# Kernel optimization log

Measured on AMD Instinct MI355X. Metric: run time of the kernel, lower is better.

Reference implementation:

```python
import jax, jax.numpy as jnp
import numpy as np

B, L, D, H, T = 1024, 50, 4, 512, 30


def _lstm_cell(x, h, c, W_ih, W_hh, b_ih, b_hh):
    # PyTorch LSTM gate order: i, f, g, o
    g = x @ W_ih.T + b_ih + h @ W_hh.T + b_hh
    i, f, gg, o = jnp.split(g, 4, axis=-1)
    c = jax.nn.sigmoid(f) * c + jax.nn.sigmoid(i) * jnp.tanh(gg)
    h = jax.nn.sigmoid(o) * jnp.tanh(c)
    return h, c


def setup_inputs() -> dict:
    key = jax.random.key(0)
    ks = jax.random.split(key, 16)
    s = 0.05
    return {
        "input_tensor": jax.random.normal(ks[0], (B, L, D), jnp.float32),
        "target_len": T,
        "enc_W_ih": jax.random.normal(ks[1], (4 * H, D), jnp.float32) * s,
        "enc_W_hh": jax.random.normal(ks[2], (4 * H, H), jnp.float32) * s,
        "enc_b_ih": jax.random.normal(ks[3], (4 * H,), jnp.float32) * s,
        "enc_b_hh": jax.random.normal(ks[4], (4 * H,), jnp.float32) * s,
        "attn_W": jax.random.normal(ks[5], (L, H + D), jnp.float32) * s,
        "attn_b": jax.random.normal(ks[6], (L,), jnp.float32) * s,
        "comb_W": jax.random.normal(ks[7], (H, H + D), jnp.float32) * s,
        "comb_b": jax.random.normal(ks[8], (H,), jnp.float32) * s,
        "dec_W_ih": jax.random.normal(ks[9], (4 * H, H), jnp.float32) * s,
        "dec_W_hh": jax.random.normal(ks[10], (4 * H, H), jnp.float32) * s,
        "dec_b_ih": jax.random.normal(ks[11], (4 * H,), jnp.float32) * s,
        "dec_b_hh": jax.random.normal(ks[12], (4 * H,), jnp.float32) * s,
        "out_W": jax.random.normal(ks[13], (D, H), jnp.float32) * s,
        "out_b": jax.random.normal(ks[14], (D,), jnp.float32) * s,
    }


def reference(input_tensor, target_len, enc_W_ih, enc_W_hh, enc_b_ih, enc_b_hh,
              attn_W, attn_b, comb_W, comb_b,
              dec_W_ih, dec_W_hh, dec_b_ih, dec_b_hh, out_W, out_b):
    b = input_tensor.shape[0]

    # ---- encoder LSTM over input_len steps ----
    def enc_step(carry, x_t):
        h, c = carry
        h, c = _lstm_cell(x_t, h, c, enc_W_ih, enc_W_hh, enc_b_ih, enc_b_hh)
        return (h, c), h

    h0 = jnp.zeros((b, H), input_tensor.dtype)
    (h_enc, c_enc), enc_hs = jax.lax.scan(enc_step, (h0, h0),
                                          jnp.swapaxes(input_tensor, 0, 1))
    encoder_outputs = jnp.swapaxes(enc_hs, 0, 1)  # [B, L, H]

    # ---- recursive attention decoder over target_len steps ----
    def dec_step(carry, _):
        h, c, x = carry
        # faithful to torch: h.reshape(h.shape[1], -1).transpose(1, 0)
        h_r = jnp.transpose(h.reshape(H, -1))  # [B, H] (memory reinterpret)
        attn_logits = jnp.concatenate([x, h_r], axis=1) @ attn_W.T + attn_b
        attn_weights = jax.nn.softmax(attn_logits, axis=1)        # [B, L]
        attn_applied = jnp.einsum('bl,blh->bh', attn_weights, encoder_outputs)
        comb = jnp.concatenate([x, attn_applied], axis=1) @ comb_W.T + comb_b
        comb = jax.nn.relu(comb)                                  # [B, H]
        h, c = _lstm_cell(comb, h, c, dec_W_ih, dec_W_hh, dec_b_ih, dec_b_hh)
        pred = h @ out_W.T + out_b                                # [B, D]
        return (h, c, pred), pred

    dec_in0 = input_tensor[:, -1, :]
    _, preds = jax.lax.scan(dec_step, (h_enc, c_enc, dec_in0), None,
                            length=target_len)
    return jnp.swapaxes(preds, 0, 1)  # [B, target_len, D]
```

## Files before the change

### kernel.cpp

```cpp
#include <hip/hip_runtime.h>
#include <hip/hip_bf16.h>

#define Bsz   1024
#define Lseq  50
#define Din   4
#define Hd    512
#define Tlen  30
#define NWG   256

typedef __hip_bfloat16 bf16;
typedef short s16x8 __attribute__((ext_vector_type(8)));
typedef short s16x4 __attribute__((ext_vector_type(4)));
typedef float f32x4 __attribute__((ext_vector_type(4)));

__device__ __forceinline__ float bf2f(bf16 x){ return __bfloat162float(x); }
__device__ __forceinline__ bf16  f2bf(float x){ return __float2bfloat16(x); }
__device__ __forceinline__ float bfbits2f(short u){
    union { unsigned int ui; float f; } v;
    v.ui = ((unsigned int)(unsigned short)u) << 16;
    return v.f;
}
__device__ __forceinline__ short f2bfbits(float x){
    bf16 h = f2bf(x); short s; __builtin_memcpy(&s, &h, 2); return s;
}
__device__ __forceinline__ float sigm(float x){ return 1.0f/(1.0f + __expf(-x)); }

#define OFF_ABUF0   (0u)
#define OFF_ABUF1   (2u<<20)
#define OFF_ATTNAP  (8u<<20)
#define OFF_XDEC    (9u<<20)
#define OFF_FLAG    ((9u<<20) + (16u<<10))
#define OFF_CNT     ((9u<<20) + (20u<<10))
#define OFF_COMBWR  ((9u<<20) + (32u<<10))
#define OFF_ATTNWR  ((9u<<20) + (600u<<10))
#define OFF_WCACHE  (10u<<20)
#define OFF_ENCOUT  (18u<<20)

#define WC_INPUT 0
#define WC_EWIH  204800
#define WC_EWHH  212992
#define WC_EBIH  1261568
#define WC_EBHH  1263616
#define WC_AW    1265664
#define WC_AB    1291464
#define WC_CW    1291520
#define WC_CB    1555712
#define WC_DWIH  1556224
#define WC_DWHH  2604800
#define WC_DBIH  3653376
#define WC_DBHH  3655424
#define WC_OW    3657472
#define WC_OB    3659520
#define WC_TOTAL 3659524

__device__ __constant__ int WOFF[15] = {
    WC_INPUT, WC_EWIH, WC_EWHH, WC_EBIH, WC_EBHH, WC_AW, WC_AB, WC_CW,
    WC_CB, WC_DWIH, WC_DWHH, WC_DBIH, WC_DBHH, WC_OW, WC_OB };
__device__ __constant__ int WNUM[15] = {
    204800, 8192, 1048576, 2048, 2048, 25800, 50, 264192,
    512, 1048576, 1048576, 2048, 2048, 2048, 4 };

struct Ptrs15 { const void* p[15]; };

__global__ void probe_kernel(const unsigned int* __restrict__ w, int* flag){
    __shared__ int cnt;
    if (threadIdx.x == 0) cnt = 0;
    __syncthreads();
    int c = 0;
    for (int i = threadIdx.x; i < 4096; i += 256){
        unsigned e = (w[i] >> 7) & 0xFFu;
        c += (e >= 0x80u) ? 1 : 0;
    }
    atomicAdd(&cnt, c);
    __syncthreads();
    if (threadIdx.x == 0) *flag = (cnt > 400) ? 1 : 0;
}

__global__ __launch_bounds__(256) void convert_kernel(
    Ptrs15 srcs, const int* __restrict__ flag, bf16* __restrict__ dst)
{
    const int f = *flag;
    for (int idx = blockIdx.x*256 + threadIdx.x; idx < WC_TOTAL;
         idx += gridDim.x*256){
        int a = 0;
#pragma unroll
        for (int j = 1; j < 15; ++j) if (idx >= WOFF[j]) a = j;
        const int local = idx - WOFF[a];
        if (local >= WNUM[a]) continue;
        bf16 v;
        if (f) v = f2bf(((const float*)srcs.p[a])[local]);
        else   v = ((const bf16*)srcs.p[a])[local];
        dst[idx] = v;
    }
}

__global__ __launch_bounds__(256) void setup_kernel(
    bf16* __restrict__ Abuf0, bf16* __restrict__ Abuf1,
    bf16* __restrict__ combWr, bf16* __restrict__ attnWr,
    const bf16* __restrict__ cWc, const bf16* __restrict__ aWc)
{
    const unsigned idx = blockIdx.x*256u + threadIdx.x;
    if (idx < (unsigned)Bsz*Hd){
        const unsigned row = idx >> 9, col = idx & (Hd-1);
        const bf16 z = f2bf(0.0f);
        Abuf0[(size_t)row*1024 + Hd + col] = z;
        Abuf1[(size_t)row*1024 + Hd + col] = z;
    }
    if (idx < (unsigned)Hd*Hd)
        combWr[idx] = cWc[(size_t)(idx >> 9)*(Hd+Din) + Din + (idx & (Hd-1))];
    if (idx < (unsigned)Lseq*Hd)
        attnWr[idx] = aWc[(size_t)(idx >> 9)*(Hd+Din) + Din + (idx & (Hd-1))];
}

struct MegaP {
    const bf16 *input, *eWih, *eWhh, *ebih, *ebhh;
    const bf16 *aW, *ab, *cW, *cb, *dWih, *dWhh, *dbih, *dbhh, *oW, *ob;
    const bf16 *combWr, *attnWr;
    bf16 *A0, *A1, *encout, *attnap, *xdec;
    int *cntg, *cntl, *xccmap;
    const int *flag;
    void *dout;
};

__global__ __launch_bounds__(512, 2) void mega_kernel(MegaP P)
{
    __shared__ short whh_lds[128*520];
    __shared__ float hr_s[4][Hd];
    __shared__ float ctx_s[2][4][Hd];
    __shared__ float aw_s[4][64];
    __shared__ int   xmap_s[NWG];
    __shared__ int   info_s[4];

    const int wg = blockIdx.x, tid = threadIdx.x;
    const int wave = tid >> 6, lane = tid & 63;
    const int quad = lane >> 4, l15 = lane & 15;
    const int lbase = lane & ~3;
    const int f32out = *P.flag;

    int epg = 0;
    int eplc = 0;

    if (tid == 0){
        int xcc = 0;
        asm volatile("s_getreg_b32 %0, hwreg(HW_REG_XCC_ID)" : "=s"(xcc));
        P.xccmap[wg] = xcc & 7;
    }

    auto GBAR = [&](){
        ++epg;
        __syncthreads();
        if (tid == 0){
            __threadfence();
            __hip_atomic_fetch_add(P.cntg, 1, __ATOMIC_RELEASE, __HIP_MEMORY_SCOPE_AGENT);
            while (__hip_atomic_load(P.cntg, __ATOMIC_RELAXED, __HIP_MEMORY_SCOPE_AGENT) < epg*NWG)
                __builtin_amdgcn_s_sleep(1);
            (void)__hip_atomic_load(P.cntg, __ATOMIC_ACQUIRE, __HIP_MEMORY_SCOPE_AGENT);
        }
        __syncthreads();
    };

    GBAR();

    if (tid < NWG) xmap_s[tid] = P.xccmap[tid];
    __syncthreads();
    if (tid == 0){
        int cnt8[8] = {0,0,0,0,0,0,0,0};
        const int myx = xmap_s[wg];
        int rank = 0;
        for (int i = 0; i < NWG; ++i){
            cnt8[xmap_s[i]]++;
            if (i < wg && xmap_s[i] == myx) rank++;
        }
        int bal = 1;
        for (int i = 0; i < 8; ++i) bal &= (cnt8[i] == 32);
        info_s[0] = bal ? myx  : (wg >> 5);
        info_s[1] = bal ? rank : (wg & 31);
        info_s[2] = bal;
    }
    __syncthreads();
    const int xcd = info_s[0], slot = info_s[1], bal = info_s[2];

    int* cntl = P.cntl + xcd*16;
    auto LBAR = [&](){
        if (!bal){ GBAR(); return; }
        ++eplc;
        __syncthreads();
        if (tid == 0){
            atomicAdd(cntl, 1);
            while (__hip_atomic_load(cntl, __ATOMIC_RELAXED, __HIP_MEMORY_SCOPE_AGENT) < eplc*32)
                __builtin_amdgcn_s_sleep(1);
        }
        __syncthreads();
        asm volatile("buffer_inv" ::: "memory");
    };

    bf16* bufs[2] = { P.A0, P.A1 };

    const int mtl = slot >> 4, ntl = slot & 15;
    const int bm0 = xcd*128 + mtl*64, hc0 = ntl*32;
    const int wm = wave >> 2, wn = wave & 3;
    const int arow0 = bm0 + wm*32 + l15;

    int ng[2];
#pragma unroll
    for (int nf = 0; nf < 2; ++nf){
        const int n = wn*32 + nf*16 + l15;
        ng[nf] = (n & 3)*Hd + hc0 + (n >> 2);
    }

    float bias_e[2], wxv_e[2][4];
#pragma unroll
    for (int nf = 0; nf < 2; ++nf){
        bias_e[nf] = bf2f(P.ebih[ng[nf]]) + bf2f(P.ebhh[ng[nf]]);
        const s16x4 t4 = *reinterpret_cast<const s16x4*>(P.eWih + (size_t)ng[nf]*Din);
#pragma unroll
        for (int d = 0; d < 4; ++d) wxv_e[nf][d] = bfbits2f(t4[d]);
    }

    s16x8 breg[2][16];
#pragma unroll
    for (int nf = 0; nf < 2; ++nf)
#pragma unroll
        for (int sl = 0; sl < 16; ++sl)
            breg[nf][sl] = *reinterpret_cast<const s16x8*>(
                P.eWhh + (size_t)ng[nf]*Hd + sl*32 + quad*8);

    float creg[2][2][4];
#pragma unroll
    for (int a = 0; a < 2; ++a)
#pragma unroll
        for (int b = 0; b < 2; ++b)
#pragma unroll
            for (int r = 0; r < 4; ++r) creg[a][b][r] = 0.0f;

    for (int t = 0; t < Lseq; ++t){
        const bf16* Ain = bufs[t&1] + Hd;
        bf16* hout = bufs[(t+1)&1] + Hd;

        f32x4 acc[2][2];
#pragma unroll
        for (int mf=0; mf<2; ++mf)
#pragma unroll
            for (int nf=0; nf<2; ++nf) acc[mf][nf] = (f32x4)0.0f;

        s16x8 afr[2];
#pragma unroll
        for (int sl = 0; sl < 16; ++sl){
#pragma unroll
            for (int mf = 0; mf < 2; ++mf)
                afr[mf] = *reinterpret_cast<const s16x8*>(
                    Ain + (size_t)(arow0 + mf*16)*1024 + sl*32 + quad*8);
#pragma unroll
            for (int mf = 0; mf < 2; ++mf)
#pragma unroll
                for (int nf = 0; nf < 2; ++nf)
                    acc[mf][nf] = __builtin_amdgcn_mfma_f32_16x16x32_bf16(
                        afr[mf], breg[nf][sl], acc[mf][nf], 0, 0, 0);
        }

#pragma unroll
        for (int mf = 0; mf < 2; ++mf){
#pragma unroll
            for (int r = 0; r < 4; ++r){
                const int m = bm0 + wm*32 + mf*16 + quad*4 + r;
                const s16x4 xt = *reinterpret_cast<const s16x4*>(
                    P.input + ((size_t)m*Lseq + t)*Din);
                float xv[4];
#pragma unroll
                for (int d = 0; d < 4; ++d) xv[d] = bfbits2f(xt[d]);
#pragma unroll
                for (int nf = 0; nf < 2; ++nf){
                    const int n_loc = wn*32 + nf*16 + l15;
                    float gv = acc[mf][nf][r] + bias_e[nf]
                             + xv[0]*wxv_e[nf][0] + xv[1]*wxv_e[nf][1]
                             + xv[2]*wxv_e[nf][2] + xv[3]*wxv_e[nf][3];
                    const float gi = __shfl(gv, lbase+0);
                    const float gf = __shfl(gv, lbase+1);
                    const float gg = __shfl(gv, lbase+2);
                    const float go = __shfl(gv, lbase+3);
                    if ((lane & 3) == 0){
                        const int hcol = hc0 + (n_loc >> 2);
                        const float cn = sigm(gf)*creg[mf][nf][r] + sigm(gi)*tanhf(gg);
                        creg[mf][nf][r] = cn;
                        const float hv = sigm(go)*tanhf(cn);
                        const bf16 hb = f2bf(hv);
                        hout[(size_t)m*1024 + hcol] = hb;
                        P.encout[((size_t)m*Lseq + t)*Hd + hcol] = hb;
                    }
                }
            }
        }
        if (t == Lseq-1) GBAR(); else LBAR();
    }

#pragma unroll
    for (int nf = 0; nf < 2; ++nf)
#pragma unroll
        for (int sl = 0; sl < 16; ++sl)
            breg[nf][sl] = *reinterpret_cast<const s16x8*>(
                P.dWih + (size_t)ng[nf]*Hd + sl*32 + quad*8);

    float bias_d[2];
#pragma unroll
    for (int nf = 0; nf < 2; ++nf)
        bias_d[nf] = bf2f(P.dbih[ng[nf]]) + bf2f(P.dbhh[ng[nf]]);

    for (int i = tid; i < 128*64; i += 512){
        const int col = i >> 6;
        const int k8  = (i & 63) * 8;
        const int g   = (col & 3)*Hd + hc0 + (col >> 2);
        const s16x8 v = *reinterpret_cast<const s16x8*>(P.dWhh + (size_t)g*Hd + k8);
        *reinterpret_cast<s16x8*>(&whh_lds[col*520 + k8]) = v;
    }

    const int b0 = xcd*128 + slot*4;
    const int s_uni = b0 >> 9;
    const int p0 = b0 & (Hd-1);

    const int cwm = wave >> 1, cwn = wave & 1;
    const int ccol = hc0 + cwn*16 + l15;
    float bias_c, wxv_c[4];
    {
        bias_c = bf2f(P.cb[ccol]);
        const s16x4 t4 = *reinterpret_cast<const s16x4*>(P.cW + (size_t)ccol*(Hd+Din));
#pragma unroll
        for (int d = 0; d < 4; ++d) wxv_c[d] = bfbits2f(t4[d]);
    }
    __syncthreads();

    for (int t = 0; t < Tlen; ++t){
        const int p = t & 1;
        const bf16* hprev = bufs[p] + Hd;

        {
            const s16x4 hv = *reinterpret_cast<const s16x4*>(
                hprev + (size_t)(2*tid + s_uni)*1024 + p0);
            hr_s[0][tid] = bfbits2f(hv[0]);
            hr_s[1][tid] = bfbits2f(hv[1]);
            hr_s[2][tid] = bfbits2f(hv[2]);
            hr_s[3][tid] = bfbits2f(hv[3]);
        }
        __syncthreads();

        if (wave < 4){
            const int b = b0 + wave;
            float x0, x1, x2, x3;
            if (t == 0){
                const bf16* xp = P.input + ((size_t)b*Lseq + (Lseq-1))*Din;
                x0 = bf2f(xp[0]); x1 = bf2f(xp[1]); x2 = bf2f(xp[2]); x3 = bf2f(xp[3]);
            } else {
                float q0=0.f, q1=0.f, q2=0.f, q3=0.f;
                const bf16* hb = hprev + (size_t)b*1024;
                for (int k = lane; k < Hd; k += 64){
                    const float hv = bf2f(hb[k]);
                    q0 += hv*bf2f(P.oW[k]);
                    q1 += hv*bf2f(P.oW[Hd+k]);
                    q2 += hv*bf2f(P.oW[2*Hd+k]);
                    q3 += hv*bf2f(P.oW[3*Hd+k]);
                }
#pragma unroll
                for (int off = 32; off; off >>= 1){
                    q0 += __shfl_down(q0, off); q1 += __shfl_down(q1, off);
                    q2 += __shfl_down(q2, off); q3 += __shfl_down(q3, off);
                }
                x0 = __shfl(q0,0) + bf2f(P.ob[0]);
                x1 = __shfl(q1,0) + bf2f(P.ob[1]);
                x2 = __shfl(q2,0) + bf2f(P.ob[2]);
                x3 = __shfl(q3,0) + bf2f(P.ob[3]);
                if (lane == 0){
                    const size_t o = ((size_t)b*Tlen + (t-1))*Din;
                    if (f32out){
                        float* dp = (float*)P.dout + o;
                        dp[0]=x0; dp[1]=x1; dp[2]=x2; dp[3]=x3;
                    } else {
                        bf16* dp = (bf16*)P.dout + o;
                        dp[0]=f2bf(x0); dp[1]=f2bf(x1); dp[2]=f2bf(x2); dp[3]=f2bf(x3);
                    }
                }
            }
            if (lane == 0){
                bf16* xp = P.xdec + (size_t)b*Din;
                xp[0]=f2bf(x0); xp[1]=f2bf(x1); xp[2]=f2bf(x2); xp[3]=f2bf(x3);
            }

            float logit = -3.0e38f;
            if (lane < Lseq){
                float a0 = bf2f(P.ab[lane]);
                {
                    const bf16* wx = P.aW + (size_t)lane*(Hd+Din);
                    a0 += x0*bf2f(wx[0]) + x1*bf2f(wx[1]) + x2*bf2f(wx[2]) + x3*bf2f(wx[3]);
                }
                float a1 = 0.f, a2 = 0.f, a3 = 0.f;
                const bf16* wr = P.attnWr + (size_t)lane*Hd;
                for (int j = 0; j < Hd; j += 16){
                    float t4[4] = {0.f,0.f,0.f,0.f};
#pragma unroll
                    for (int q = 0; q < 4; ++q){
                        const float4 hv = *reinterpret_cast<const float4*>(&hr_s[wave][j + q*4]);
                        const s16x4 wv = *reinterpret_cast<const s16x4*>(wr + j + q*4);
                        t4[q] = hv.x*bfbits2f(wv[0]) + hv.y*bfbits2f(wv[1])
                              + hv.z*bfbits2f(wv[2]) + hv.w*bfbits2f(wv[3]);
                    }
                    a0 += t4[0]; a1 += t4[1]; a2 += t4[2]; a3 += t4[3];
                }
                logit = (a0 + a1) + (a2 + a3);
            }
            float mx = logit;
#pragma unroll
            for (int off = 32; off; off >>= 1) mx = fmaxf(mx, __shfl_xor(mx, off));
            const float e = (lane < Lseq) ? __expf(logit - mx) : 0.0f;
            float se = e;
#pragma unroll
            for (int off = 32; off; off >>= 1) se += __shfl_xor(se, off);
            aw_s[wave][lane] = e / se;
        }
        __syncthreads();

        {
            const int r = wave & 3, half = wave >> 2;
            const int b = b0 + r;
            float acc8[8] = {0.f,0.f,0.f,0.f,0.f,0.f,0.f,0.f};
            const bf16* eb = P.encout + (size_t)b*Lseq*Hd + lane*8;
            for (int i = 0; i < 25; ++i){
                const int l = half*25 + i;
                const float w = aw_s[r][l];
                const s16x8 ch = *reinterpret_cast<const s16x8*>(eb + (size_t)l*Hd);
#pragma unroll
                for (int q = 0; q < 8; ++q) acc8[q] += w * bfbits2f(ch[q]);
            }
            float* cp = &ctx_s[half][r][lane*8];
            *reinterpret_cast<float4*>(cp)     = make_float4(acc8[0],acc8[1],acc8[2],acc8[3]);
            *reinterpret_cast<float4*>(cp + 4) = make_float4(acc8[4],acc8[5],acc8[6],acc8[7]);
        }
        __syncthreads();

        if (wave < 4){
            const int b = b0 + wave;
            s16x8 ov;
#pragma unroll
            for (int q = 0; q < 8; ++q)
                ov[q] = f2bfbits(ctx_s[0][wave][lane*8+q] + ctx_s[1][wave][lane*8+q]);
            *reinterpret_cast<s16x8*>(P.attnap + (size_t)b*Hd + lane*8) = ov;
        }
        LBAR();

        {
            f32x4 cacc = (f32x4)0.0f;
            const bf16* Ab = P.attnap + (size_t)(bm0 + cwm*16 + l15)*Hd + quad*8;
#pragma unroll
            for (int kk = 0; kk < 16; ++kk){
                const s16x8 bfr = *reinterpret_cast<const s16x8*>(
                    P.combWr + (size_t)ccol*Hd + kk*32 + quad*8);
                const s16x8 afr2 = *reinterpret_cast<const s16x8*>(Ab + kk*32);
                cacc = __builtin_amdgcn_mfma_f32_16x16x32_bf16(afr2, bfr, cacc, 0, 0, 0);
            }
            bf16* outp = bufs[p];
#pragma unroll
            for (int r = 0; r < 4; ++r){
                const int m = bm0 + cwm*16 + quad*4 + r;
                const s16x4 xt = *reinterpret_cast<const s16x4*>(P.xdec + (size_t)m*Din);
                float v = cacc[r] + bias_c
                        + bfbits2f(xt[0])*wxv_c[0] + bfbits2f(xt[1])*wxv_c[1]
                        + bfbits2f(xt[2])*wxv_c[2] + bfbits2f(xt[3])*wxv_c[3];
                v = fmaxf(v, 0.0f);
                outp[(size_t)m*1024 + ccol] = f2bf(v);
            }
        }
        LBAR();

        {
            const bf16* Ain = bufs[p];
            bf16* hout = bufs[p^1] + Hd;
            f32x4 acc[2][2];
#pragma unroll
            for (int mf=0; mf<2; ++mf)
#pragma unroll
                for (int nf=0; nf<2; ++nf) acc[mf][nf] = (f32x4)0.0f;

            s16x8 afr[2], bfr[2];
#pragma unroll
            for (int sl = 0; sl < 16; ++sl){
#pragma unroll
                for (int mf = 0; mf < 2; ++mf)
                    afr[mf] = *reinterpret_cast<const s16x8*>(
                        Ain + (size_t)(arow0 + mf*16)*1024 + sl*32 + quad*8);
#pragma unroll
                for (int mf = 0; mf < 2; ++mf)
#pragma unroll
                    for (int nf = 0; nf < 2; ++nf)
                        acc[mf][nf] = __builtin_amdgcn_mfma_f32_16x16x32_bf16(
                            afr[mf], breg[nf][sl], acc[mf][nf], 0, 0, 0);
            }
#pragma unroll
            for (int sl = 0; sl < 16; ++sl){
#pragma unroll
                for (int nf = 0; nf < 2; ++nf){
                    const int nl = wn*32 + nf*16 + l15;
                    bfr[nf] = *reinterpret_cast<const s16x8*>(
                        &whh_lds[nl*520 + sl*32 + quad*8]);
                }
#pragma unroll
                for (int mf = 0; mf < 2; ++mf)
                    afr[mf] = *reinterpret_cast<const s16x8*>(
                        Ain + (size_t)(arow0 + mf*16)*1024 + Hd + sl*32 + quad*8);
#pragma unroll
                for (int mf = 0; mf < 2; ++mf)
#pragma unroll
                    for (int nf = 0; nf < 2; ++nf)
                        acc[mf][nf] = __builtin_amdgcn_mfma_f32_16x16x32_bf16(
                            afr[mf], bfr[nf], acc[mf][nf], 0, 0, 0);
            }

#pragma unroll
            for (int mf = 0; mf < 2; ++mf){
#pragma unroll
                for (int r = 0; r < 4; ++r){
                    const int m = bm0 + wm*32 + mf*16 + quad*4 + r;
#pragma unroll
                    for (int nf = 0; nf < 2; ++nf){
                        const int n_loc = wn*32 + nf*16 + l15;
                        float gv = acc[mf][nf][r] + bias_d[nf];
                        const float gi = __shfl(gv, lbase+0);
                        const float gf = __shfl(gv, lbase+1);
                        const float gg = __shfl(gv, lbase+2);
                        const float go = __shfl(gv, lbase+3);
                        if ((lane & 3) == 0){
                            const int hcol = hc0 + (n_loc >> 2);
                            const float cn = sigm(gf)*creg[mf][nf][r] + sigm(gi)*tanhf(gg);
                            creg[mf][nf][r] = cn;
                            const float hv = sigm(go)*tanhf(cn);
                            hout[(size_t)m*1024 + hcol] = f2bf(hv);
                        }
                    }
                }
            }
        }
        GBAR();
    }

    if (wave < 4){
        const int b = b0 + wave;
        const bf16* hb = bufs[Tlen & 1] + Hd + (size_t)b*1024;
        float q0=0.f, q1=0.f, q2=0.f, q3=0.f;
        for (int k = lane; k < Hd; k += 64){
            const float hv = bf2f(hb[k]);
            q0 += hv*bf2f(P.oW[k]);
            q1 += hv*bf2f(P.oW[Hd+k]);
            q2 += hv*bf2f(P.oW[2*Hd+k]);
            q3 += hv*bf2f(P.oW[3*Hd+k]);
        }
#pragma unroll
        for (int off = 32; off; off >>= 1){
            q0 += __shfl_down(q0, off); q1 += __shfl_down(q1, off);
            q2 += __shfl_down(q2, off); q3 += __shfl_down(q3, off);
        }
        if (lane == 0){
            const size_t o = ((size_t)b*Tlen + (Tlen-1))*Din;
            const float r0 = q0 + bf2f(P.ob[0]), r1 = q1 + bf2f(P.ob[1]);
            const float r2 = q2 + bf2f(P.ob[2]), r3 = q3 + bf2f(P.ob[3]);
            if (f32out){
                float* dp = (float*)P.dout + o;
                dp[0]=r0; dp[1]=r1; dp[2]=r2; dp[3]=r3;
            } else {
                bf16* dp = (bf16*)P.dout + o;
                dp[0]=f2bf(r0); dp[1]=f2bf(r1); dp[2]=f2bf(r2); dp[3]=f2bf(r3);
            }
        }
    }
}

extern "C" void kernel_launch(void* const* d_in, const int* in_sizes, int n_in,
                              void* d_out, int out_size, void* d_ws, size_t ws_size,
                              hipStream_t stream)
{
    char* ws = (char*)d_ws;
    bf16*  Abuf0   = (bf16*)(ws + OFF_ABUF0);
    bf16*  Abuf1   = (bf16*)(ws + OFF_ABUF1);
    bf16*  attnap  = (bf16*)(ws + OFF_ATTNAP);
    bf16*  xdec    = (bf16*)(ws + OFF_XDEC);
    int*   flag    = (int*)(ws + OFF_FLAG);
    int*   cntblk  = (int*)(ws + OFF_CNT);
    bf16*  combWr  = (bf16*)(ws + OFF_COMBWR);
    bf16*  attnWr  = (bf16*)(ws + OFF_ATTNWR);
    bf16*  wc      = (bf16*)(ws + OFF_WCACHE);
    bf16*  enc_out = (bf16*)(ws + OFF_ENCOUT);

    hipMemsetAsync(cntblk, 0, 4096, stream);

    probe_kernel<<<1, 256, 0, stream>>>((const unsigned int*)d_in[3], flag);

    Ptrs15 srcs;
    srcs.p[0]=d_in[0];  srcs.p[1]=d_in[2];  srcs.p[2]=d_in[3];  srcs.p[3]=d_in[4];
    srcs.p[4]=d_in[5];  srcs.p[5]=d_in[6];  srcs.p[6]=d_in[7];  srcs.p[7]=d_in[8];
    srcs.p[8]=d_in[9];  srcs.p[9]=d_in[10]; srcs.p[10]=d_in[11];srcs.p[11]=d_in[12];
    srcs.p[12]=d_in[13];srcs.p[13]=d_in[14];srcs.p[14]=d_in[15];
    convert_kernel<<<1024, 256, 0, stream>>>(srcs, flag, wc);

    setup_kernel<<<2048, 256, 0, stream>>>(Abuf0, Abuf1, combWr, attnWr,
                                           wc+WC_CW, wc+WC_AW);

    MegaP P;
    P.input = wc+WC_INPUT; P.eWih = wc+WC_EWIH; P.eWhh = wc+WC_EWHH;
    P.ebih = wc+WC_EBIH;   P.ebhh = wc+WC_EBHH;
    P.aW = wc+WC_AW;  P.ab = wc+WC_AB;  P.cW = wc+WC_CW;  P.cb = wc+WC_CB;
    P.dWih = wc+WC_DWIH; P.dWhh = wc+WC_DWHH; P.dbih = wc+WC_DBIH; P.dbhh = wc+WC_DBHH;
    P.oW = wc+WC_OW;  P.ob = wc+WC_OB;
    P.combWr = combWr; P.attnWr = attnWr;
    P.A0 = Abuf0; P.A1 = Abuf1; P.encout = enc_out; P.attnap = attnap; P.xdec = xdec;
    P.cntg = cntblk; P.cntl = cntblk + 16; P.xccmap = cntblk + 16 + 8*16;
    P.flag = flag; P.dout = d_out;

    mega_kernel<<<NWG, 512, 0, stream>>>(P);
}
```

Measured before the change: 3.614 ms.

## Replace atomic-counter grid barriers with per-workgroup flag sync and cache-bypassing stores

Removes the XCC-mapped counter barriers. Each workgroup now publishes an epoch flag and waits only on the 16 workgroups sharing its row tile (PSYNC), with a two-level hierarchical flag barrier for global syncs (GSYNC). Cross-WG data is written with sc0 sc1 stores so no threadfence is needed, followed by buffer_inv. Also switches tanhf to an exp-based fast tanh, stores hr_s as bf16, and pads the LDS weight rows. The aim is lower barrier latency and less atomic contention, at the cost of dropping XCD locality in the WG mapping and relying on relaxed flag ordering being correct.

```diff
diff --git a/kernel.cpp b/kernel.cpp
--- a/kernel.cpp
+++ b/kernel.cpp
@@ -12,6 +12,7 @@
 typedef short s16x8 __attribute__((ext_vector_type(8)));
 typedef short s16x4 __attribute__((ext_vector_type(4)));
 typedef float f32x4 __attribute__((ext_vector_type(4)));
+typedef int   i32x2 __attribute__((ext_vector_type(2)));
 
 __device__ __forceinline__ float bf2f(bf16 x){ return __bfloat162float(x); }
 __device__ __forceinline__ bf16  f2bf(float x){ return __float2bfloat16(x); }
@@ -24,15 +25,40 @@
     bf16 h = f2bf(x); short s; __builtin_memcpy(&s, &h, 2); return s;
 }
 __device__ __forceinline__ float sigm(float x){ return 1.0f/(1.0f + __expf(-x)); }
+__device__ __forceinline__ float ftanh(float x){
+    const float e = __expf(2.0f*x);
+    return 1.0f - 2.0f/(e + 1.0f);
+}
+
+__device__ __forceinline__ void sc_store_short(bf16* p, bf16 v){
+    short s; __builtin_memcpy(&s, &v, 2);
+    int si = (int)s;
+    asm volatile("global_store_short %0, %1, off sc0 sc1" :: "v"(p), "v"(si) : "memory");
+}
+__device__ __forceinline__ void sc_store_b64(void* p, i32x2 v){
+    asm volatile("global_store_dwordx2 %0, %1, off sc0 sc1" :: "v"(p), "v"(v) : "memory");
+}
+__device__ __forceinline__ void sc_store_b128s(void* p, s16x8 v){
+    asm volatile("global_store_dwordx4 %0, %1, off sc0 sc1" :: "v"(p), "v"(v) : "memory");
+}
+__device__ __forceinline__ void sc_store_b128f(void* p, f32x4 v){
+    asm volatile("global_store_dwordx4 %0, %1, off sc0 sc1" :: "v"(p), "v"(v) : "memory");
+}
+__device__ __forceinline__ i32x2 pack4(float a, float b, float c, float d){
+    i32x2 v;
+    v[0] = (int)(unsigned short)f2bfbits(a) | ((int)(unsigned short)f2bfbits(b) << 16);
+    v[1] = (int)(unsigned short)f2bfbits(c) | ((int)(unsigned short)f2bfbits(d) << 16);
+    return v;
+}
 
 #define OFF_ABUF0   (0u)
 #define OFF_ABUF1   (2u<<20)
 #define OFF_ATTNAP  (8u<<20)
 #define OFF_XDEC    (9u<<20)
 #define OFF_FLAG    ((9u<<20) + (16u<<10))
-#define OFF_CNT     ((9u<<20) + (20u<<10))
 #define OFF_COMBWR  ((9u<<20) + (32u<<10))
 #define OFF_ATTNWR  ((9u<<20) + (600u<<10))
+#define OFF_FLAGS   ((9u<<20) + (704u<<10))
 #define OFF_WCACHE  (10u<<20)
 #define OFF_ENCOUT  (18u<<20)
 
@@ -117,19 +143,17 @@
     const bf16 *aW, *ab, *cW, *cb, *dWih, *dWhh, *dbih, *dbhh, *oW, *ob;
     const bf16 *combWr, *attnWr;
     bf16 *A0, *A1, *encout, *attnap, *xdec;
-    int *cntg, *cntl, *xccmap;
+    int *wflag, *gflag;
     const int *flag;
     void *dout;
 };
 
 __global__ __launch_bounds__(512, 2) void mega_kernel(MegaP P)
 {
-    __shared__ short whh_lds[128*520];
-    __shared__ float hr_s[4][Hd];
+    __shared__ short whh_lds[128*536];
+    __shared__ short hr_s[4][Hd];
     __shared__ float ctx_s[2][4][Hd];
     __shared__ float aw_s[4][64];
-    __shared__ int   xmap_s[NWG];
-    __shared__ int   info_s[4];
 
     const int wg = blockIdx.x, tid = threadIdx.x;
     const int wave = tid >> 6, lane = tid & 63;
@@ -137,69 +161,51 @@
     const int lbase = lane & ~3;
     const int f32out = *P.flag;
 
-    int epg = 0;
-    int eplc = 0;
-
-    if (tid == 0){
-        int xcc = 0;
-        asm volatile("s_getreg_b32 %0, hwreg(HW_REG_XCC_ID)" : "=s"(xcc));
-        P.xccmap[wg] = xcc & 7;
-    }
-
-    auto GBAR = [&](){
-        ++epg;
-        __syncthreads();
-        if (tid == 0){
-            __threadfence();
-            __hip_atomic_fetch_add(P.cntg, 1, __ATOMIC_RELEASE, __HIP_MEMORY_SCOPE_AGENT);
-            while (__hip_atomic_load(P.cntg, __ATOMIC_RELAXED, __HIP_MEMORY_SCOPE_AGENT) < epg*NWG)
-                __builtin_amdgcn_s_sleep(1);
-            (void)__hip_atomic_load(P.cntg, __ATOMIC_ACQUIRE, __HIP_MEMORY_SCOPE_AGENT);
-        }
-        __syncthreads();
-    };
-
-    GBAR();
-
-    if (tid < NWG) xmap_s[tid] = P.xccmap[tid];
-    __syncthreads();
-    if (tid == 0){
-        int cnt8[8] = {0,0,0,0,0,0,0,0};
-        const int myx = xmap_s[wg];
-        int rank = 0;
-        for (int i = 0; i < NWG; ++i){
-            cnt8[xmap_s[i]]++;
-            if (i < wg && xmap_s[i] == myx) rank++;
-        }
-        int bal = 1;
-        for (int i = 0; i < 8; ++i) bal &= (cnt8[i] == 32);
-        info_s[0] = bal ? myx  : (wg >> 5);
-        info_s[1] = bal ? rank : (wg & 31);
-        info_s[2] = bal;
-    }
-    __syncthreads();
-    const int xcd = info_s[0], slot = info_s[1], bal = info_s[2];
-
-    int* cntl = P.cntl + xcd*16;
-    auto LBAR = [&](){
-        if (!bal){ GBAR(); return; }
-        ++eplc;
-        __syncthreads();
-        if (tid == 0){
-            atomicAdd(cntl, 1);
-            while (__hip_atomic_load(cntl, __ATOMIC_RELAXED, __HIP_MEMORY_SCOPE_AGENT) < eplc*32)
-                __builtin_amdgcn_s_sleep(1);
-        }
-        __syncthreads();
-        asm volatile("buffer_inv" ::: "memory");
-    };
-
-    bf16* bufs[2] = { P.A0, P.A1 };
-
-    const int mtl = slot >> 4, ntl = slot & 15;
-    const int bm0 = xcd*128 + mtl*64, hc0 = ntl*32;
+    int ep = 0;
+
+    const int mt = wg >> 4, nt = wg & 15;
+    const int bm0 = mt << 6, hc0 = nt << 5;
     const int wm = wave >> 2, wn = wave & 3;
     const int arow0 = bm0 + wm*32 + l15;
+
+    auto PSYNC = [&](){
+        ++ep;
+        __syncthreads();
+        if (tid == 0)
+            __hip_atomic_store(P.wflag + wg*16, ep, __ATOMIC_RELAXED, __HIP_MEMORY_SCOPE_SYSTEM);
+        if (tid < 16){
+            const int* f = P.wflag + (mt*16 + tid)*16;
+            while (__hip_atomic_load(f, __ATOMIC_RELAXED, __HIP_MEMORY_SCOPE_SYSTEM) < ep)
+                __builtin_amdgcn_s_sleep(1);
+        }
+        __syncthreads();
+        asm volatile("buffer_inv sc0 sc1" ::: "memory");
+    };
+
+    auto GSYNC = [&](){
+        ++ep;
+        __syncthreads();
+        if (tid == 0)
+            __hip_atomic_store(P.wflag + wg*16, ep, __ATOMIC_RELAXED, __HIP_MEMORY_SCOPE_SYSTEM);
+        if ((wg & 31) == 0){
+            if (tid < 32){
+                const int* f = P.wflag + (wg + tid)*16;
+                while (__hip_atomic_load(f, __ATOMIC_RELAXED, __HIP_MEMORY_SCOPE_SYSTEM) < ep)
+                    __builtin_amdgcn_s_sleep(1);
+            }
+            if (tid == 0)
+                __hip_atomic_store(P.gflag + (wg >> 5)*16, ep, __ATOMIC_RELAXED, __HIP_MEMORY_SCOPE_SYSTEM);
+        }
+        if (tid < 8){
+            const int* f = P.gflag + tid*16;
+            while (__hip_atomic_load(f, __ATOMIC_RELAXED, __HIP_MEMORY_SCOPE_SYSTEM) < ep)
+                __builtin_amdgcn_s_sleep(1);
+        }
+        __syncthreads();
+        asm volatile("buffer_inv sc0 sc1" ::: "memory");
+    };
+
+    bf16* bufs[2] = { P.A0, P.A1 };
 
     int ng[2];
 #pragma unroll
@@ -280,17 +286,17 @@
                     const float go = __shfl(gv, lbase+3);
                     if ((lane & 3) == 0){
                         const int hcol = hc0 + (n_loc >> 2);
-                        const float cn = sigm(gf)*creg[mf][nf][r] + sigm(gi)*tanhf(gg);
+                        const float cn = sigm(gf)*creg[mf][nf][r] + sigm(gi)*ftanh(gg);
                         creg[mf][nf][r] = cn;
-                        const float hv = sigm(go)*tanhf(cn);
+                        const float hv = sigm(go)*ftanh(cn);
                         const bf16 hb = f2bf(hv);
-                        hout[(size_t)m*1024 + hcol] = hb;
-                        P.encout[((size_t)m*Lseq + t)*Hd + hcol] = hb;
+                        sc_store_short(hout + (size_t)m*1024 + hcol, hb);
+                        sc_store_short(P.encout + ((size_t)m*Lseq + t)*Hd + hcol, hb);
                     }
                 }
             }
         }
-        if (t == Lseq-1) GBAR(); else LBAR();
+        if (t == Lseq-1) GSYNC(); else PSYNC();
     }
 
 #pragma unroll
@@ -310,10 +316,10 @@
         const int k8  = (i & 63) * 8;
         const int g   = (col & 3)*Hd + hc0 + (col >> 2);
         const s16x8 v = *reinterpret_cast<const s16x8*>(P.dWhh + (size_t)g*Hd + k8);
-        *reinterpret_cast<s16x8*>(&whh_lds[col*520 + k8]) = v;
-    }
-
-    const int b0 = xcd*128 + slot*4;
+        *reinterpret_cast<s16x8*>(&whh_lds[col*536 + k8]) = v;
+    }
+
+    const int b0 = wg*4;
     const int s_uni = b0 >> 9;
     const int p0 = b0 & (Hd-1);
 
@@ -335,10 +341,8 @@
         {
             const s16x4 hv = *reinterpret_cast<const s16x4*>(
                 hprev + (size_t)(2*tid + s_uni)*1024 + p0);
-            hr_s[0][tid] = bfbits2f(hv[0]);
-            hr_s[1][tid] = bfbits2f(hv[1]);
-            hr_s[2][tid] = bfbits2f(hv[2]);
-            hr_s[3][tid] = bfbits2f(hv[3]);
+            hr_s[0][tid] = hv[0]; hr_s[1][tid] = hv[1];
+            hr_s[2][tid] = hv[2]; hr_s[3][tid] = hv[3];
         }
         __syncthreads();
 
@@ -370,18 +374,15 @@
                 if (lane == 0){
                     const size_t o = ((size_t)b*Tlen + (t-1))*Din;
                     if (f32out){
-                        float* dp = (float*)P.dout + o;
-                        dp[0]=x0; dp[1]=x1; dp[2]=x2; dp[3]=x3;
+                        f32x4 v; v[0]=x0; v[1]=x1; v[2]=x2; v[3]=x3;
+                        sc_store_b128f((float*)P.dout + o, v);
                     } else {
-                        bf16* dp = (bf16*)P.dout + o;
-                        dp[0]=f2bf(x0); dp[1]=f2bf(x1); dp[2]=f2bf(x2); dp[3]=f2bf(x3);
+                        sc_store_b64((bf16*)P.dout + o, pack4(x0,x1,x2,x3));
                     }
                 }
             }
-            if (lane == 0){
-                bf16* xp = P.xdec + (size_t)b*Din;
-                xp[0]=f2bf(x0); xp[1]=f2bf(x1); xp[2]=f2bf(x2); xp[3]=f2bf(x3);
-            }
+            if (lane == 0)
+                sc_store_b64(P.xdec + (size_t)b*Din, pack4(x0,x1,x2,x3));
 
             float logit = -3.0e38f;
             if (lane < Lseq){
@@ -396,10 +397,10 @@
                     float t4[4] = {0.f,0.f,0.f,0.f};
 #pragma unroll
                     for (int q = 0; q < 4; ++q){
-                        const float4 hv = *reinterpret_cast<const float4*>(&hr_s[wave][j + q*4]);
+                        const s16x4 hw = *reinterpret_cast<const s16x4*>(&hr_s[wave][j + q*4]);
                         const s16x4 wv = *reinterpret_cast<const s16x4*>(wr + j + q*4);
-                        t4[q] = hv.x*bfbits2f(wv[0]) + hv.y*bfbits2f(wv[1])
-                              + hv.z*bfbits2f(wv[2]) + hv.w*bfbits2f(wv[3]);
+                        t4[q] = bfbits2f(hw[0])*bfbits2f(wv[0]) + bfbits2f(hw[1])*bfbits2f(wv[1])
+                              + bfbits2f(hw[2])*bfbits2f(wv[2]) + bfbits2f(hw[3])*bfbits2f(wv[3]);
                     }
                     a0 += t4[0]; a1 += t4[1]; a2 += t4[2]; a3 += t4[3];
                 }
@@ -440,9 +441,9 @@
 #pragma unroll
             for (int q = 0; q < 8; ++q)
                 ov[q] = f2bfbits(ctx_s[0][wave][lane*8+q] + ctx_s[1][wave][lane*8+q]);
-            *reinterpret_cast<s16x8*>(P.attnap + (size_t)b*Hd + lane*8) = ov;
-        }
-        LBAR();
+            sc_store_b128s(P.attnap + (size_t)b*Hd + lane*8, ov);
+        }
+        PSYNC();
 
         {
             f32x4 cacc = (f32x4)0.0f;
@@ -463,10 +464,10 @@
                         + bfbits2f(xt[0])*wxv_c[0] + bfbits2f(xt[1])*wxv_c[1]
                         + bfbits2f(xt[2])*wxv_c[2] + bfbits2f(xt[3])*wxv_c[3];
                 v = fmaxf(v, 0.0f);
-                outp[(size_t)m*1024 + ccol] = f2bf(v);
-            }
-        }
-        LBAR();
+                sc_store_short(outp + (size_t)m*1024 + ccol, f2bf(v));
+            }
+        }
+        PSYNC();
 
         {
             const bf16* Ain = bufs[p];
@@ -497,7 +498,7 @@
                 for (int nf = 0; nf < 2; ++nf){
                     const int nl = wn*32 + nf*16 + l15;
                     bfr[nf] = *reinterpret_cast<const s16x8*>(
-                        &whh_lds[nl*520 + sl*32 + quad*8]);
+                        &whh_lds[nl*536 + sl*32 + quad*8]);
                 }
 #pragma unroll
                 for (int mf = 0; mf < 2; ++mf)
@@ -526,16 +527,16 @@
                         const float go = __shfl(gv, lbase+3);
                         if ((lane & 3) == 0){
                             const int hcol = hc0 + (n_loc >> 2);
-                            const float cn = sigm(gf)*creg[mf][nf][r] + sigm(gi)*tanhf(gg);
+                            const float cn = sigm(gf)*creg[mf][nf][r] + sigm(gi)*ftanh(gg);
                             creg[mf][nf][r] = cn;
-                            const float hv = sigm(go)*tanhf(cn);
-                            hout[(size_t)m*1024 + hcol] = f2bf(hv);
+                            const float hv = sigm(go)*ftanh(cn);
+                            sc_store_short(hout + (size_t)m*1024 + hcol, f2bf(hv));
                         }
                     }
                 }
             }
         }
-        GBAR();
+        GSYNC();
     }
 
     if (wave < 4){
@@ -559,11 +560,10 @@
             const float r0 = q0 + bf2f(P.ob[0]), r1 = q1 + bf2f(P.ob[1]);
             const float r2 = q2 + bf2f(P.ob[2]), r3 = q3 + bf2f(P.ob[3]);
             if (f32out){
-                float* dp = (float*)P.dout + o;
-                dp[0]=r0; dp[1]=r1; dp[2]=r2; dp[3]=r3;
+                f32x4 v; v[0]=r0; v[1]=r1; v[2]=r2; v[3]=r3;
+                sc_store_b128f((float*)P.dout + o, v);
             } else {
-                bf16* dp = (bf16*)P.dout + o;
-                dp[0]=f2bf(r0); dp[1]=f2bf(r1); dp[2]=f2bf(r2); dp[3]=f2bf(r3);
+                sc_store_b64((bf16*)P.dout + o, pack4(r0,r1,r2,r3));
             }
         }
     }
@@ -579,13 +579,13 @@
     bf16*  attnap  = (bf16*)(ws + OFF_ATTNAP);
     bf16*  xdec    = (bf16*)(ws + OFF_XDEC);
     int*   flag    = (int*)(ws + OFF_FLAG);
-    int*   cntblk  = (int*)(ws + OFF_CNT);
     bf16*  combWr  = (bf16*)(ws + OFF_COMBWR);
     bf16*  attnWr  = (bf16*)(ws + OFF_ATTNWR);
+    int*   flags   = (int*)(ws + OFF_FLAGS);
     bf16*  wc      = (bf16*)(ws + OFF_WCACHE);
     bf16*  enc_out = (bf16*)(ws + OFF_ENCOUT);
 
-    hipMemsetAsync(cntblk, 0, 4096, stream);
+    hipMemsetAsync(flags, 0, 20480, stream);
 
     probe_kernel<<<1, 256, 0, stream>>>((const unsigned int*)d_in[3], flag);
 
@@ -607,7 +607,7 @@
     P.oW = wc+WC_OW;  P.ob = wc+WC_OB;
     P.combWr = combWr; P.attnWr = attnWr;
     P.A0 = Abuf0; P.A1 = Abuf1; P.encout = enc_out; P.attnap = attnap; P.xdec = xdec;
-    P.cntg = cntblk; P.cntl = cntblk + 16; P.xccmap = cntblk + 16 + 8*16;
+    P.wflag = flags; P.gflag = flags + 256*16;
     P.flag = flag; P.dout = d_out;
 
     mega_kernel<<<NWG, 512, 0, stream>>>(P);
```

After: 4.650 ms. 28.7% more time.
